# Optimization experiments

Measured on AMD Instinct MI355X. Metric: run time of the kernel, lower is better.

## Reference

```python
import jax, jax.numpy as jnp
import numpy as np

N = 20000       # nodes
E = 320000      # edges (avg in-degree 16)
IN_DIM = 128
HID = 64
HEADS = 4
NUM_GRAPHS = 128
N_CLASSES = 10


def setup_inputs() -> dict:
    key = jax.random.key(0)
    ks = jax.random.split(key, 8)
    h = jax.random.normal(ks[0], (N, IN_DIM), jnp.float32)
    src = jax.random.randint(ks[1], (E,), 0, N)
    dst = jax.random.randint(ks[2], (E,), 0, N)
    graph_ids = jnp.sort(jax.random.randint(ks[3], (N,), 0, NUM_GRAPHS))
    # DotGatConv fc weights (no bias in DGL DotGatConv), classifier Linear w/ bias
    W1 = jax.random.normal(ks[4], (IN_DIM, HID * HEADS), jnp.float32) / np.sqrt(IN_DIM).astype(np.float32)
    W2 = jax.random.normal(ks[5], (HID * HEADS, HID), jnp.float32) / np.sqrt(HID * HEADS).astype(np.float32)
    Wc = jax.random.normal(ks[6], (HID, N_CLASSES), jnp.float32) / np.sqrt(HID).astype(np.float32)
    bc = jnp.zeros((N_CLASSES,), jnp.float32)
    return {"h": h, "src": src, "dst": dst, "graph_ids": graph_ids,
            "W1": W1, "W2": W2, "Wc": Wc, "bc": bc}


def dot_gat(x, src, dst, W, num_heads):
    """DGL DotGatConv: scaled dot-product attention over graph edges."""
    n = x.shape[0]
    d = W.shape[1] // num_heads
    ft = (x @ W).reshape(n, num_heads, d)          # [N,H,D]
    hs = ft[src]                                    # [E,H,D] source feats
    hd = ft[dst]                                    # [E,H,D] dest feats
    e = (hs * hd).sum(-1) / jnp.sqrt(jnp.float32(d))  # [E,H] edge scores
    # edge softmax over incoming edges per destination node (stable)
    m = jax.ops.segment_max(e, dst, num_segments=n)    # [N,H]
    ee = jnp.exp(e - m[dst])                           # [E,H]
    den = jax.ops.segment_sum(ee, dst, num_segments=n)[dst]  # [E,H]
    a = ee / den
    # aggregate attention-weighted source messages at destination
    return jax.ops.segment_sum(hs * a[..., None], dst, num_segments=n)  # [N,H,D]


def reference(h, src, dst, graph_ids, W1, W2, Wc, bc):
    n = h.shape[0]
    x = jax.nn.relu(dot_gat(h, src, dst, W1, HEADS)).reshape(n, -1)   # [N, HID*HEADS]
    x = jax.nn.relu(dot_gat(x, src, dst, W2, 1)).reshape(n, -1)       # [N, HID]
    # AvgPooling: mean of node features per graph
    cnt = jax.ops.segment_sum(jnp.ones((n,), x.dtype), graph_ids, num_segments=NUM_GRAPHS)
    pooled = jax.ops.segment_sum(x, graph_ids, num_segments=NUM_GRAPHS) / jnp.maximum(cnt, 1.0)[:, None]
    return pooled @ Wc + bc                                            # [NUM_GRAPHS, N_CLASSES]
```

## Files before the change

### kernel.cpp

```cpp
#include <hip/hip_runtime.h>
#include <hip/hip_bf16.h>

typedef __attribute__((ext_vector_type(8))) __bf16 bf16x8;
typedef __attribute__((ext_vector_type(8))) unsigned short ushort8;
typedef __attribute__((ext_vector_type(4))) float floatx4;

#define N_NODES   20000
#define N_EDGES   320000
#define IN_DIM    128
#define HID       64
#define HEADS     4
#define NUM_GRAPHS 128
#define N_CLASSES 10
#define BCAP      128

__device__ inline float cvt_load(const void* p, int i, int isb) {
    return isb ? __bfloat162float(((const __hip_bfloat16*)p)[i]) : ((const float*)p)[i];
}

__device__ inline unsigned short bf16bits(float v) {
    return __builtin_bit_cast(unsigned short, __float2bfloat16(v));
}

__device__ inline unsigned pack2(float a, float b) {
    return (unsigned)bf16bits(a) | ((unsigned)bf16bits(b) << 16);
}

__device__ inline floatx4 unpack4(uint2 u) {
    floatx4 f;
    f.x = __uint_as_float(u.x << 16);
    f.y = __uint_as_float(u.x & 0xffff0000u);
    f.z = __uint_as_float(u.y << 16);
    f.w = __uint_as_float(u.y & 0xffff0000u);
    return f;
}

__global__ void init_kernel(const unsigned int* hw, int nwords, int* flag,
                            unsigned int* cnt, float* pooled) {
    int b = blockIdx.x;
    if (b == 0) {
        __shared__ int s_bad;
        if (threadIdx.x == 0) s_bad = 0;
        __syncthreads();
        int bad = 0;
        for (int i = threadIdx.x; i < nwords; i += 256) {
            float v = __uint_as_float(hw[i]);
            if (!(fabsf(v) <= 1e20f)) bad = 1;
        }
        if (bad) atomicOr(&s_bad, 1);
        __syncthreads();
        if (threadIdx.x == 0) *flag = s_bad;
    } else {
        int i = (b - 1) * 256 + threadIdx.x;
        if (i < N_NODES) cnt[i] = 0u;
        else if (i < N_NODES + NUM_GRAPHS * HID) pooled[i - N_NODES] = 0.f;
    }
}

__global__ void prep_kernel(const void* W1, const void* W2, const void* Wc, const void* bc,
                            unsigned short* W1t, unsigned short* W2t, float* Wcf, float* bcf,
                            const int* __restrict__ src, const int* __restrict__ dst,
                            int* __restrict__ cnt, int* __restrict__ bucket,
                            const int* flag) {
    int b = blockIdx.x;
    const int n1 = IN_DIM * HID * HEADS;
    const int n2 = HID * HEADS * HID;
    const int n3 = HID * N_CLASSES;
    const int n4 = N_CLASSES;
    if (b < 195) {
        int i = b * 256 + threadIdx.x;
        int isb = *flag;
        if (i < n1) {
            int k = i >> 8, n = i & 255;
            W1t[n * 128 + k] = bf16bits(cvt_load(W1, i, isb));
        } else if (i < n1 + n2) {
            int j = i - n1;
            int k = j >> 6, n = j & 63;
            W2t[n * 256 + k] = bf16bits(cvt_load(W2, j, isb));
        } else if (i < n1 + n2 + n3) {
            int j = i - n1 - n2;
            Wcf[j] = cvt_load(Wc, j, isb);
        } else if (i < n1 + n2 + n3 + n4) {
            int j = i - n1 - n2 - n3;
            bcf[j] = cvt_load(bc, j, isb);
        }
    } else {
        int e = (b - 195) * 256 + threadIdx.x;
        if (e < N_EDGES) {
            int d = dst[e];
            int pos = atomicAdd(&cnt[d], 1);
            if (pos < BCAP) bucket[d * BCAP + pos] = src[e];
        }
    }
}

__global__ __launch_bounds__(256) void gemm1_kernel(const void* __restrict__ h_any,
                                                    const unsigned short* __restrict__ Bt,
                                                    unsigned short* __restrict__ C, int M,
                                                    const int* flag) {
    int wave = threadIdx.x >> 6;
    int lane = threadIdx.x & 63;
    int q = lane >> 4, r = lane & 15;
    int m0 = blockIdx.x * 64;
    int n0 = wave * 64;
    floatx4 acc[4][4] = {};
    bf16x8 bfrag[4][4];
#pragma unroll
    for (int ni = 0; ni < 4; ++ni)
#pragma unroll
        for (int kk = 0; kk < 4; ++kk)
            bfrag[ni][kk] = *(const bf16x8*)(Bt + (n0 + ni * 16 + r) * 128 + kk * 32 + q * 8);
    if (*flag) {
        const unsigned short* A = (const unsigned short*)h_any;
#pragma unroll
        for (int kk = 0; kk < 4; ++kk) {
            bf16x8 afrag[4];
#pragma unroll
            for (int mi = 0; mi < 4; ++mi) {
                int row = m0 + mi * 16 + r;
                bf16x8 a = {};
                if (row < M) a = *(const bf16x8*)(A + row * 128 + kk * 32 + q * 8);
                afrag[mi] = a;
            }
#pragma unroll
            for (int mi = 0; mi < 4; ++mi)
#pragma unroll
                for (int ni = 0; ni < 4; ++ni)
                    acc[mi][ni] = __builtin_amdgcn_mfma_f32_16x16x32_bf16(afrag[mi], bfrag[ni][kk], acc[mi][ni], 0, 0, 0);
        }
    } else {
        const float* A = (const float*)h_any;
#pragma unroll
        for (int kk = 0; kk < 4; ++kk) {
            bf16x8 afrag[4];
#pragma unroll
            for (int mi = 0; mi < 4; ++mi) {
                int row = m0 + mi * 16 + r;
                bf16x8 a = {};
                if (row < M) {
                    const floatx4* p = (const floatx4*)(A + row * 128 + kk * 32 + q * 8);
                    floatx4 f0 = p[0], f1 = p[1];
                    ushort8 u;
                    u[0] = bf16bits(f0.x); u[1] = bf16bits(f0.y);
                    u[2] = bf16bits(f0.z); u[3] = bf16bits(f0.w);
                    u[4] = bf16bits(f1.x); u[5] = bf16bits(f1.y);
                    u[6] = bf16bits(f1.z); u[7] = bf16bits(f1.w);
                    a = __builtin_bit_cast(bf16x8, u);
                }
                afrag[mi] = a;
            }
#pragma unroll
            for (int mi = 0; mi < 4; ++mi)
#pragma unroll
                for (int ni = 0; ni < 4; ++ni)
                    acc[mi][ni] = __builtin_amdgcn_mfma_f32_16x16x32_bf16(afrag[mi], bfrag[ni][kk], acc[mi][ni], 0, 0, 0);
        }
    }
#pragma unroll
    for (int mi = 0; mi < 4; ++mi)
#pragma unroll
        for (int rr = 0; rr < 4; ++rr) {
            int row = m0 + mi * 16 + q * 4 + rr;
            if (row < M) {
#pragma unroll
                for (int ni = 0; ni < 4; ++ni)
                    C[row * 256 + n0 + ni * 16 + r] = bf16bits(acc[mi][ni][rr]);
            }
        }
}

__global__ __launch_bounds__(512) void attn4proj_kernel(const unsigned short* __restrict__ ft,
                                                        const int* __restrict__ cnt,
                                                        const int* __restrict__ bucket,
                                                        const unsigned short* __restrict__ W2t,
                                                        unsigned short* __restrict__ ft2) {
    __shared__ unsigned short x1t[8][256];
    int w    = threadIdx.x >> 6;
    int lane = threadIdx.x & 63;
    int dstv = blockIdx.x * 8 + w;
    floatx4 hd = unpack4(*(const uint2*)(ft + dstv * 256 + lane * 4));
    int deg  = min(cnt[dstv], BCAP);
    int base = dstv * BCAP;
    float l = 0.f;
    floatx4 acc = {0.f, 0.f, 0.f, 0.f};
    int i0 = 0;
    for (; i0 + 4 <= deg; i0 += 4) {
        int sn0 = bucket[base + i0],     sn1 = bucket[base + i0 + 1];
        int sn2 = bucket[base + i0 + 2], sn3 = bucket[base + i0 + 3];
        uint2 r0 = *(const uint2*)(ft + sn0 * 256 + lane * 4);
        uint2 r1 = *(const uint2*)(ft + sn1 * 256 + lane * 4);
        uint2 r2 = *(const uint2*)(ft + sn2 * 256 + lane * 4);
        uint2 r3 = *(const uint2*)(ft + sn3 * 256 + lane * 4);
        floatx4 h0 = unpack4(r0), h1 = unpack4(r1), h2 = unpack4(r2), h3 = unpack4(r3);
        float p0 = h0.x * hd.x + h0.y * hd.y + h0.z * hd.z + h0.w * hd.w;
        float p1 = h1.x * hd.x + h1.y * hd.y + h1.z * hd.z + h1.w * hd.w;
        float p2 = h2.x * hd.x + h2.y * hd.y + h2.z * hd.z + h2.w * hd.w;
        float p3 = h3.x * hd.x + h3.y * hd.y + h3.z * hd.z + h3.w * hd.w;
        p0 += __shfl_xor(p0, 1); p1 += __shfl_xor(p1, 1); p2 += __shfl_xor(p2, 1); p3 += __shfl_xor(p3, 1);
        p0 += __shfl_xor(p0, 2); p1 += __shfl_xor(p1, 2); p2 += __shfl_xor(p2, 2); p3 += __shfl_xor(p3, 2);
        p0 += __shfl_xor(p0, 4); p1 += __shfl_xor(p1, 4); p2 += __shfl_xor(p2, 4); p3 += __shfl_xor(p3, 4);
        p0 += __shfl_xor(p0, 8); p1 += __shfl_xor(p1, 8); p2 += __shfl_xor(p2, 8); p3 += __shfl_xor(p3, 8);
        float w0 = __expf(p0 * 0.125f);
        float w1 = __expf(p1 * 0.125f);
        float w2 = __expf(p2 * 0.125f);
        float w3 = __expf(p3 * 0.125f);
        l += (w0 + w1) + (w2 + w3);
        acc.x += w0 * h0.x + w1 * h1.x + w2 * h2.x + w3 * h3.x;
        acc.y += w0 * h0.y + w1 * h1.y + w2 * h2.y + w3 * h3.y;
        acc.z += w0 * h0.z + w1 * h1.z + w2 * h2.z + w3 * h3.z;
        acc.w += w0 * h0.w + w1 * h1.w + w2 * h2.w + w3 * h3.w;
    }
    for (; i0 < deg; ++i0) {
        int sn = bucket[base + i0];
        floatx4 hs = unpack4(*(const uint2*)(ft + sn * 256 + lane * 4));
        float p = hs.x * hd.x + hs.y * hd.y + hs.z * hd.z + hs.w * hd.w;
        p += __shfl_xor(p, 1); p += __shfl_xor(p, 2);
        p += __shfl_xor(p, 4); p += __shfl_xor(p, 8);
        float wgt = __expf(p * 0.125f);
        l += wgt;
        acc.x += wgt * hs.x; acc.y += wgt * hs.y;
        acc.z += wgt * hs.z; acc.w += wgt * hs.w;
    }
    float inv = (l > 0.f) ? 1.f / l : 0.f;
    unsigned* xr = (unsigned*)&x1t[w][lane * 4];
    xr[0] = pack2(fmaxf(acc.x * inv, 0.f), fmaxf(acc.y * inv, 0.f));
    xr[1] = pack2(fmaxf(acc.z * inv, 0.f), fmaxf(acc.w * inv, 0.f));
    __syncthreads();
    if (w < 4) {
        int q = lane >> 4, r = lane & 15;
        floatx4 pacc = {0.f, 0.f, 0.f, 0.f};
#pragma unroll
        for (int kk = 0; kk < 8; ++kk) {
            bf16x8 bfrag = *(const bf16x8*)(W2t + (w * 16 + r) * 256 + kk * 32 + q * 8);
            bf16x8 afrag = {};
            if (r < 8) afrag = *(const bf16x8*)(&x1t[r][kk * 32 + q * 8]);
            pacc = __builtin_amdgcn_mfma_f32_16x16x32_bf16(afrag, bfrag, pacc, 0, 0, 0);
        }
#pragma unroll
        for (int rr = 0; rr < 4; ++rr) {
            int row = q * 4 + rr;
            if (row < 8)
                ft2[(blockIdx.x * 8 + row) * 64 + w * 16 + r] = bf16bits(pacc[rr]);
        }
    }
}

__global__ __launch_bounds__(256) void attn1pool_kernel(const unsigned short* __restrict__ ft,
                                                        const int* __restrict__ cnt,
                                                        const int* __restrict__ bucket,
                                                        const int* __restrict__ gid,
                                                        float* __restrict__ pooled) {
    int dstv = blockIdx.x * 4 + (threadIdx.x >> 6);
    int lane = threadIdx.x & 63;
    int g = lane >> 4, s = lane & 15;
    int hbase = s * 4;
    floatx4 hd = unpack4(*(const uint2*)(ft + dstv * 64 + hbase));
    int deg  = min(cnt[dstv], BCAP);
    int base = dstv * BCAP;
    float l = 0.f;
    floatx4 acc = {0.f, 0.f, 0.f, 0.f};
    int i0 = 0;
    for (; i0 + 8 <= deg; i0 += 8) {
        int ia = i0 + g, ib = i0 + 4 + g;
        int sa = bucket[base + ia], sb = bucket[base + ib];
        uint2 ra = *(const uint2*)(ft + sa * 64 + hbase);
        uint2 rb = *(const uint2*)(ft + sb * 64 + hbase);
        floatx4 ha = unpack4(ra), hb = unpack4(rb);
        float pa = ha.x * hd.x + ha.y * hd.y + ha.z * hd.z + ha.w * hd.w;
        float pb = hb.x * hd.x + hb.y * hd.y + hb.z * hd.z + hb.w * hd.w;
        pa += __shfl_xor(pa, 1); pb += __shfl_xor(pb, 1);
        pa += __shfl_xor(pa, 2); pb += __shfl_xor(pb, 2);
        pa += __shfl_xor(pa, 4); pb += __shfl_xor(pb, 4);
        pa += __shfl_xor(pa, 8); pb += __shfl_xor(pb, 8);
        float wa = __expf(pa * 0.125f);
        float wb = __expf(pb * 0.125f);
        l += wa + wb;
        acc.x += wa * ha.x + wb * hb.x;
        acc.y += wa * ha.y + wb * hb.y;
        acc.z += wa * ha.z + wb * hb.z;
        acc.w += wa * ha.w + wb * hb.w;
    }
    for (; i0 < deg; i0 += 4) {
        int i = i0 + g;
        bool valid = (i < deg);
        int sn = valid ? bucket[base + i] : 0;
        floatx4 hs = unpack4(*(const uint2*)(ft + sn * 64 + hbase));
        float p = hs.x * hd.x + hs.y * hd.y + hs.z * hd.z + hs.w * hd.w;
        p += __shfl_xor(p, 1); p += __shfl_xor(p, 2);
        p += __shfl_xor(p, 4); p += __shfl_xor(p, 8);
        float wgt = valid ? __expf(p * 0.125f) : 0.f;
        l += wgt;
        acc.x += wgt * hs.x; acc.y += wgt * hs.y;
        acc.z += wgt * hs.z; acc.w += wgt * hs.w;
    }
    l += __shfl_xor(l, 16); l += __shfl_xor(l, 32);
    acc.x += __shfl_xor(acc.x, 16); acc.x += __shfl_xor(acc.x, 32);
    acc.y += __shfl_xor(acc.y, 16); acc.y += __shfl_xor(acc.y, 32);
    acc.z += __shfl_xor(acc.z, 16); acc.z += __shfl_xor(acc.z, 32);
    acc.w += __shfl_xor(acc.w, 16); acc.w += __shfl_xor(acc.w, 32);
    float inv = (l > 0.f) ? 1.f / l : 0.f;
    if (g == 0) {
        int gg = gid[dstv];
        float* pp = pooled + gg * HID + hbase;
        atomicAdd(pp + 0, fmaxf(acc.x * inv, 0.f));
        atomicAdd(pp + 1, fmaxf(acc.y * inv, 0.f));
        atomicAdd(pp + 2, fmaxf(acc.z * inv, 0.f));
        atomicAdd(pp + 3, fmaxf(acc.w * inv, 0.f));
    }
}

__global__ __launch_bounds__(64) void classify_kernel(const float* __restrict__ pooled,
                                                      const int* __restrict__ gid,
                                                      const float* __restrict__ Wc,
                                                      const float* __restrict__ bc,
                                                      void* out, const int* flag) {
    __shared__ int s_lo, s_hi;
    int g = blockIdx.x;
    int d = threadIdx.x;
    if (d == 0) {
        int lo = 0, hi = N_NODES;
        while (lo < hi) { int m = (lo + hi) >> 1; if (gid[m] < g) lo = m + 1; else hi = m; }
        s_lo = lo;
        int lo2 = lo, hi2 = N_NODES;
        while (lo2 < hi2) { int m = (lo2 + hi2) >> 1; if (gid[m] < g + 1) lo2 = m + 1; else hi2 = m; }
        s_hi = lo2;
    }
    __syncthreads();
    int cntg = s_hi - s_lo;
    float mean = (cntg > 0) ? pooled[g * HID + d] / (float)cntg : 0.f;
    for (int cls = 0; cls < N_CLASSES; ++cls) {
        float p = mean * Wc[d * N_CLASSES + cls];
#pragma unroll
        for (int o = 1; o < 64; o <<= 1) p += __shfl_xor(p, o);
        if (d == 0) {
            float r = p + bc[cls];
            if (*flag) ((__hip_bfloat16*)out)[g * N_CLASSES + cls] = __float2bfloat16(r);
            else       ((float*)out)[g * N_CLASSES + cls] = r;
        }
    }
}

static inline size_t align256(size_t x) { return (x + 255) & ~size_t(255); }

extern "C" void kernel_launch(void* const* d_in, const int* in_sizes, int n_in,
                              void* d_out, int out_size, void* d_ws, size_t ws_size,
                              hipStream_t stream) {
    const void* h_raw  = d_in[0];
    const int*  src    = (const int*)d_in[1];
    const int*  dst    = (const int*)d_in[2];
    const int*  gid    = (const int*)d_in[3];
    const void* W1_raw = d_in[4];
    const void* W2_raw = d_in[5];
    const void* Wc_raw = d_in[6];
    const void* bc_raw = d_in[7];

    char* w = (char*)d_ws;
    int*  flag     = (int*)w;                      w += 256;
    int*  cnt      = (int*)w;                      w += align256(N_NODES * 4);
    int*  bucket   = (int*)w;                      w += align256((size_t)N_NODES * BCAP * 4);
    unsigned short* W1t = (unsigned short*)w;      w += align256(256 * 128 * 2);
    unsigned short* W2t = (unsigned short*)w;      w += align256(64 * 256 * 2);
    float* Wcf     = (float*)w;                    w += align256(HID * N_CLASSES * 4);
    float* bcf     = (float*)w;                    w += 256;
    unsigned short* ft1  = (unsigned short*)w;     w += align256((size_t)N_NODES * 256 * 2);
    unsigned short* ft2  = (unsigned short*)w;     w += align256((size_t)N_NODES * HID * 2);
    float* pooled  = (float*)w;                    w += align256((size_t)NUM_GRAPHS * HID * 4);

    hipLaunchKernelGGL(init_kernel,
                       dim3(1 + (N_NODES + NUM_GRAPHS * HID + 255) / 256), dim3(256), 0, stream,
                       (const unsigned int*)h_raw, 4096, flag,
                       (unsigned int*)cnt, pooled);

    hipLaunchKernelGGL(prep_kernel, dim3(195 + 1250), dim3(256), 0, stream,
                       W1_raw, W2_raw, Wc_raw, bc_raw, W1t, W2t, Wcf, bcf,
                       src, dst, cnt, bucket, flag);

    hipLaunchKernelGGL(gemm1_kernel, dim3((N_NODES + 63) / 64), dim3(256), 0, stream,
                       h_raw, W1t, ft1, N_NODES, flag);

    hipLaunchKernelGGL(attn4proj_kernel, dim3(N_NODES / 8), dim3(512), 0, stream,
                       ft1, cnt, bucket, W2t, ft2);

    hipLaunchKernelGGL(attn1pool_kernel, dim3(N_NODES / 4), dim3(256), 0, stream,
                       ft2, cnt, bucket, gid, pooled);

    hipLaunchKernelGGL(classify_kernel, dim3(NUM_GRAPHS), dim3(64), 0, stream,
                       pooled, gid, Wcf, bcf, d_out, flag);
}
```

Before: 206.7 us.

## Replace atomic graph pooling with per-node stores and segmented pool-classify kernel

The second attention layer now writes each node's ReLU output to a dense fp32 buffer instead of doing float atomicAdds into per-graph pooled sums. A new pool+classify kernel finds each graph's contiguous node range with binary search over the sorted graph ids, reduces it with four waves, then applies the classifier. This removes heavy atomic contention on only 128×64 addresses, and the zeroing of the pooled buffer goes away. In exchange it adds a 5 MB write and re-read, and the final reduction runs on only 128 blocks.

```diff
diff --git a/kernel.cpp b/kernel.cpp
--- a/kernel.cpp
+++ b/kernel.cpp
@@ -36,7 +36,7 @@
 }
 
 __global__ void init_kernel(const unsigned int* hw, int nwords, int* flag,
-                            unsigned int* cnt, float* pooled) {
+                            unsigned int* cnt, int n1) {
     int b = blockIdx.x;
     if (b == 0) {
         __shared__ int s_bad;
@@ -52,8 +52,7 @@
         if (threadIdx.x == 0) *flag = s_bad;
     } else {
         int i = (b - 1) * 256 + threadIdx.x;
-        if (i < N_NODES) cnt[i] = 0u;
-        else if (i < N_NODES + NUM_GRAPHS * HID) pooled[i - N_NODES] = 0.f;
+        if (i < n1) cnt[i] = 0u;
     }
 }
 
@@ -245,11 +244,10 @@
     }
 }
 
-__global__ __launch_bounds__(256) void attn1pool_kernel(const unsigned short* __restrict__ ft,
-                                                        const int* __restrict__ cnt,
-                                                        const int* __restrict__ bucket,
-                                                        const int* __restrict__ gid,
-                                                        float* __restrict__ pooled) {
+__global__ __launch_bounds__(256) void attn_h1_kernel(const unsigned short* __restrict__ ft,
+                                                      const int* __restrict__ cnt,
+                                                      const int* __restrict__ bucket,
+                                                      float* __restrict__ out) {
     int dstv = blockIdx.x * 4 + (threadIdx.x >> 6);
     int lane = threadIdx.x & 63;
     int g = lane >> 4, s = lane & 15;
@@ -300,24 +298,22 @@
     acc.w += __shfl_xor(acc.w, 16); acc.w += __shfl_xor(acc.w, 32);
     float inv = (l > 0.f) ? 1.f / l : 0.f;
     if (g == 0) {
-        int gg = gid[dstv];
-        float* pp = pooled + gg * HID + hbase;
-        atomicAdd(pp + 0, fmaxf(acc.x * inv, 0.f));
-        atomicAdd(pp + 1, fmaxf(acc.y * inv, 0.f));
-        atomicAdd(pp + 2, fmaxf(acc.z * inv, 0.f));
-        atomicAdd(pp + 3, fmaxf(acc.w * inv, 0.f));
-    }
-}
-
-__global__ __launch_bounds__(64) void classify_kernel(const float* __restrict__ pooled,
-                                                      const int* __restrict__ gid,
-                                                      const float* __restrict__ Wc,
-                                                      const float* __restrict__ bc,
-                                                      void* out, const int* flag) {
+        floatx4 o = {fmaxf(acc.x * inv, 0.f), fmaxf(acc.y * inv, 0.f),
+                     fmaxf(acc.z * inv, 0.f), fmaxf(acc.w * inv, 0.f)};
+        *(floatx4*)(out + dstv * 64 + hbase) = o;
+    }
+}
+
+__global__ __launch_bounds__(256) void poolclass_kernel(const float* __restrict__ x,
+                                                        const int* __restrict__ gid,
+                                                        const float* __restrict__ Wc,
+                                                        const float* __restrict__ bc,
+                                                        void* out, const int* flag) {
     __shared__ int s_lo, s_hi;
+    __shared__ float part[4][64];
     int g = blockIdx.x;
-    int d = threadIdx.x;
-    if (d == 0) {
+    int tid = threadIdx.x;
+    if (tid == 0) {
         int lo = 0, hi = N_NODES;
         while (lo < hi) { int m = (lo + hi) >> 1; if (gid[m] < g) lo = m + 1; else hi = m; }
         s_lo = lo;
@@ -326,16 +322,25 @@
         s_hi = lo2;
     }
     __syncthreads();
-    int cntg = s_hi - s_lo;
-    float mean = (cntg > 0) ? pooled[g * HID + d] / (float)cntg : 0.f;
-    for (int cls = 0; cls < N_CLASSES; ++cls) {
-        float p = mean * Wc[d * N_CLASSES + cls];
-#pragma unroll
-        for (int o = 1; o < 64; o <<= 1) p += __shfl_xor(p, o);
-        if (d == 0) {
-            float r = p + bc[cls];
-            if (*flag) ((__hip_bfloat16*)out)[g * N_CLASSES + cls] = __float2bfloat16(r);
-            else       ((float*)out)[g * N_CLASSES + cls] = r;
+    int lo = s_lo, hi = s_hi;
+    int d = tid & 63, w = tid >> 6;
+    float sum = 0.f;
+    for (int n = lo + w; n < hi; n += 4) sum += x[n * 64 + d];
+    part[w][d] = sum;
+    __syncthreads();
+    if (w == 0) {
+        float tot = part[0][d] + part[1][d] + part[2][d] + part[3][d];
+        int cntg = hi - lo;
+        float mean = (cntg > 0) ? tot / (float)cntg : 0.f;
+        for (int cls = 0; cls < N_CLASSES; ++cls) {
+            float p = mean * Wc[d * N_CLASSES + cls];
+#pragma unroll
+            for (int o = 1; o < 64; o <<= 1) p += __shfl_xor(p, o);
+            if (d == 0) {
+                float r = p + bc[cls];
+                if (*flag) ((__hip_bfloat16*)out)[g * N_CLASSES + cls] = __float2bfloat16(r);
+                else       ((float*)out)[g * N_CLASSES + cls] = r;
+            }
         }
     }
 }
@@ -364,12 +369,11 @@
     float* bcf     = (float*)w;                    w += 256;
     unsigned short* ft1  = (unsigned short*)w;     w += align256((size_t)N_NODES * 256 * 2);
     unsigned short* ft2  = (unsigned short*)w;     w += align256((size_t)N_NODES * HID * 2);
-    float* pooled  = (float*)w;                    w += align256((size_t)NUM_GRAPHS * HID * 4);
-
-    hipLaunchKernelGGL(init_kernel,
-                       dim3(1 + (N_NODES + NUM_GRAPHS * HID + 255) / 256), dim3(256), 0, stream,
+    float* x2      = (float*)w;                    w += align256((size_t)N_NODES * HID * 4);
+
+    hipLaunchKernelGGL(init_kernel, dim3(1 + (N_NODES + 255) / 256), dim3(256), 0, stream,
                        (const unsigned int*)h_raw, 4096, flag,
-                       (unsigned int*)cnt, pooled);
+                       (unsigned int*)cnt, N_NODES);
 
     hipLaunchKernelGGL(prep_kernel, dim3(195 + 1250), dim3(256), 0, stream,
                        W1_raw, W2_raw, Wc_raw, bc_raw, W1t, W2t, Wcf, bcf,
@@ -381,9 +385,9 @@
     hipLaunchKernelGGL(attn4proj_kernel, dim3(N_NODES / 8), dim3(512), 0, stream,
                        ft1, cnt, bucket, W2t, ft2);
 
-    hipLaunchKernelGGL(attn1pool_kernel, dim3(N_NODES / 4), dim3(256), 0, stream,
-                       ft2, cnt, bucket, gid, pooled);
-
-    hipLaunchKernelGGL(classify_kernel, dim3(NUM_GRAPHS), dim3(64), 0, stream,
-                       pooled, gid, Wcf, bcf, d_out, flag);
-}
+    hipLaunchKernelGGL(attn_h1_kernel, dim3(N_NODES / 4), dim3(256), 0, stream,
+                       ft2, cnt, bucket, x2);
+
+    hipLaunchKernelGGL(poolclass_kernel, dim3(NUM_GRAPHS), dim3(256), 0, stream,
+                       x2, gid, Wcf, bcf, d_out, flag);
+}
```

New measurement: 177.7 us. -14.0%, faster.
